# Performance work log

Hardware: AMD Instinct MI355X
Metric: run time of the kernel (lower is better)

Reference implementation:

```python
import jax, jax.numpy as jnp
import numpy as np

B, S, D, H, DH, F = 4, 2048, 1024, 16, 64, 4096
EPS = 1e-5


def setup_inputs() -> dict:
    key = jax.random.key(0)
    ks = jax.random.split(key, 8)
    std = 0.02
    return {
        "src": jax.random.normal(ks[0], (B, S, D), dtype=jnp.float32),
        # per-head Q/K/V projections, stacked: [H, D, DH]
        "Wq": jax.random.normal(ks[1], (H, D, DH), dtype=jnp.float32) * std,
        "bq": jnp.zeros((H, DH), dtype=jnp.float32),
        "Wk": jax.random.normal(ks[2], (H, D, DH), dtype=jnp.float32) * std,
        "bk": jnp.zeros((H, DH), dtype=jnp.float32),
        "Wv": jax.random.normal(ks[3], (H, D, DH), dtype=jnp.float32) * std,
        "bv": jnp.zeros((H, DH), dtype=jnp.float32),
        "Wo": jax.random.normal(ks[4], (H * DH, D), dtype=jnp.float32) * std,
        "bo": jnp.zeros((D,), dtype=jnp.float32),
        "ln1_w": jnp.ones((D,), dtype=jnp.float32),
        "ln1_b": jnp.zeros((D,), dtype=jnp.float32),
        "W1": jax.random.normal(ks[5], (D, F), dtype=jnp.float32) * std,
        "b1": jnp.zeros((F,), dtype=jnp.float32),
        "W2": jax.random.normal(ks[6], (F, D), dtype=jnp.float32) * std,
        "b2": jnp.zeros((D,), dtype=jnp.float32),
        "ln2_w": jnp.ones((D,), dtype=jnp.float32),
        "ln2_b": jnp.zeros((D,), dtype=jnp.float32),
    }


def _layernorm(x, w, b):
    m = jnp.mean(x, axis=-1, keepdims=True)
    v = jnp.mean(jnp.square(x - m), axis=-1, keepdims=True)
    return (x - m) * jax.lax.rsqrt(v + EPS) * w + b


def reference(src, Wq, bq, Wk, bk, Wv, bv, Wo, bo, ln1_w, ln1_b, W1, b1, W2, b2, ln2_w, ln2_b):
    # Per-head projections, batched over heads: [B,H,S,DH]
    q = jnp.einsum('bsd,hde->bhse', src, Wq) + bq[None, :, None, :]
    k = jnp.einsum('bsd,hde->bhse', src, Wk) + bk[None, :, None, :]
    v = jnp.einsum('bsd,hde->bhse', src, Wv) + bv[None, :, None, :]
    scale = jnp.asarray(DH, src.dtype) ** 0.5
    scores = jnp.einsum('bhqe,bhke->bhqk', q, k) / scale  # [B,H,S,S]
    attn = jax.nn.softmax(scores, axis=-1)
    ctx = jnp.einsum('bhqk,bhke->bhqe', attn, v)  # [B,H,S,DH]
    # concat heads along feature dim (matches torch.cat over head outputs)
    ctx = ctx.transpose(0, 2, 1, 3).reshape(src.shape[0], src.shape[1], H * DH)
    attn_out = ctx @ Wo + bo
    x = _layernorm(src + attn_out, ln1_w, ln1_b)
    ffn = jax.nn.relu(x @ W1 + b1) @ W2 + b2
    return _layernorm(x + ffn, ln2_w, ln2_b)
```

## Files before the change

kernel.cpp:

```cpp
#include <hip/hip_runtime.h>
#include <stdint.h>


typedef unsigned short u16;
typedef __attribute__((ext_vector_type(8))) short short8;
typedef __attribute__((ext_vector_type(4))) float f32x4;
typedef __attribute__((ext_vector_type(16))) float f32x16;

__device__ __forceinline__ u16 f2bf(float f) {
  union { float f; unsigned u; } v; v.f = f;
  unsigned r = (v.u + 0x7fffu + ((v.u >> 16) & 1u)) >> 16;
  return (u16)r;
}

__device__ __forceinline__ void gl_lds16(const u16* g, u16* l) {
  __builtin_amdgcn_global_load_lds(
      (const __attribute__((address_space(1))) unsigned int*)g,
      (__attribute__((address_space(3))) unsigned int*)l, 16, 0, 0);
}

__device__ __forceinline__ unsigned cvtpk(float lo, float hi) {
  unsigned r;
  asm("v_cvt_pk_bf16_f32 %0, %1, %2" : "=v"(r) : "v"(lo), "v"(hi));
  return r;
}
__device__ __forceinline__ void pl32_swap(unsigned& a, unsigned& b) {
  asm("v_permlane32_swap_b32 %0, %1" : "+v"(a), "+v"(b));
}


__global__ __launch_bounds__(256) void transpose_cast(const float* __restrict__ W,
                                                      u16* __restrict__ WT,
                                                      int K, int N) {
  __shared__ u16 T[64 * 72];
  const int tid = threadIdx.x;
  const long n0 = (long)blockIdx.x * 64, k0 = (long)blockIdx.y * 64;
#pragma unroll
  for (int i = 0; i < 4; i++) {
    int c = tid + i * 256;
    int kr = c >> 4, nc = (c & 15) * 4;
    float4 v = *(const float4*)(W + (k0 + kr) * N + n0 + nc);
    T[(nc + 0) * 72 + kr] = f2bf(v.x);
    T[(nc + 1) * 72 + kr] = f2bf(v.y);
    T[(nc + 2) * 72 + kr] = f2bf(v.z);
    T[(nc + 3) * 72 + kr] = f2bf(v.w);
  }
  __syncthreads();
#pragma unroll
  for (int i = 0; i < 2; i++) {
    int c = tid + i * 256;
    int nr = c >> 3, kc = (c & 7) * 8;
    *(uint4*)(WT + (n0 + nr) * K + k0 + kc) = *(const uint4*)(T + nr * 72 + kc);
  }
}

__global__ __launch_bounds__(256) void transpose_cast_qkv(const float* __restrict__ Wq,
                                                          const float* __restrict__ Wk,
                                                          const float* __restrict__ Wv,
                                                          u16* __restrict__ WT) {
  __shared__ u16 T[64 * 72];
  const int tid = threadIdx.x;
  const int n0 = blockIdx.x * 64, k0 = blockIdx.y * 64;
  const float* W = (n0 < 1024) ? Wq : (n0 < 2048 ? Wk : Wv);
  const int h = (n0 & 1023) >> 6;
#pragma unroll
  for (int i = 0; i < 4; i++) {
    int c = tid + i * 256;
    int kr = c >> 4, ec = (c & 15) * 4;
    float4 v = *(const float4*)(W + ((long)h * 1024 + k0 + kr) * 64 + ec);
    T[(ec + 0) * 72 + kr] = f2bf(v.x);
    T[(ec + 1) * 72 + kr] = f2bf(v.y);
    T[(ec + 2) * 72 + kr] = f2bf(v.z);
    T[(ec + 3) * 72 + kr] = f2bf(v.w);
  }
  __syncthreads();
#pragma unroll
  for (int i = 0; i < 2; i++) {
    int c = tid + i * 256;
    int nr = c >> 3, kc = (c & 7) * 8;
    *(uint4*)(WT + ((long)(n0 + nr)) * 1024 + k0 + kc) = *(const uint4*)(T + nr * 72 + kc);
  }
}

__global__ __launch_bounds__(256) void cast_bf16(const float* __restrict__ x, u16* __restrict__ y) {
  const long i = ((long)blockIdx.x * 256 + threadIdx.x) * 8;
  float4 a = *(const float4*)(x + i);
  float4 b = *(const float4*)(x + i + 4);
  uint4 o;
  o.x = (unsigned)f2bf(a.x) | ((unsigned)f2bf(a.y) << 16);
  o.y = (unsigned)f2bf(a.z) | ((unsigned)f2bf(a.w) << 16);
  o.z = (unsigned)f2bf(b.x) | ((unsigned)f2bf(b.y) << 16);
  o.w = (unsigned)f2bf(b.z) | ((unsigned)f2bf(b.w) << 16);
  *(uint4*)(y + i) = o;
}

__global__ __launch_bounds__(256) void build_bcat(const float* __restrict__ bq,
                                                  const float* __restrict__ bk,
                                                  const float* __restrict__ bv,
                                                  float* __restrict__ bcat) {
  int i = blockIdx.x * 256 + threadIdx.x;
  const float* s = (i < 1024) ? bq : (i < 2048 ? bk : bv);
  bcat[i] = s[i & 1023];
}

#define GEMM_SETUP                                                                 \
  __shared__ __align__(16) u16 Bs[2][4096];                                        \
  const int tid = threadIdx.x;                                                     \
  const int wave = tid >> 6, lane = tid & 63, quad = lane >> 4, l15 = lane & 15;   \
  const int wm = (wave >> 1) * 64, wn = (wave & 1) * 64;                           \
  const int id = blockIdx.x, xcd = id & 7, ii = id >> 3;                           \
  const long m0 = (long)(xcd * 8 + (ii & 7)) * 128, n0 = (long)(ii >> 3) * 128;    \
  const int srow = tid >> 2, sc = (tid & 3) ^ ((srow >> 1) & 3);                   \
  const u16* Bg = B + (n0 + srow) * K + sc * 8;                                    \
  const int cq = quad ^ ((l15 >> 1) & 3);                                          \
  const u16* Ap = A + (m0 + wm + l15) * K + quad * 8;                              \
  f32x4 acc[4][4] = {};

#define GEMM_KLOOP                                                                 \
  gl_lds16(Bg, &Bs[0][tid * 8]);                                                   \
  gl_lds16(Bg + (long)64 * K, &Bs[0][tid * 8 + 2048]);                             \
  short8 afc[4], afn[4];                                                           \
  _Pragma("unroll") for (int t = 0; t < 4; t++)                                    \
      afc[t] = *(const short8*)(Ap + (long)t * 16 * K);                            \
  for (int k0 = 0; k0 < K; k0 += 32) {                                             \
    __syncthreads();    \
    const int cur = (k0 >> 5) & 1;                                                 \
    if (k0 + 32 < K) {                                                             \
      gl_lds16(Bg + k0 + 32, &Bs[cur ^ 1][tid * 8]);                               \
      gl_lds16(Bg + (long)64 * K + k0 + 32, &Bs[cur ^ 1][tid * 8 + 2048]);         \
      _Pragma("unroll") for (int t = 0; t < 4; t++)                                \
          afn[t] = *(const short8*)(Ap + (long)t * 16 * K + k0 + 32);              \
    }                                                                              \
    short8 bfr[4];                                                                 \
    _Pragma("unroll") for (int t = 0; t < 4; t++)                                  \
        bfr[t] = *(const short8*)(&Bs[cur][(wn + t * 16 + l15) * 32 + cq * 8]);    \
    _Pragma("unroll") for (int i = 0; i < 4; i++)                                  \
        _Pragma("unroll") for (int j = 0; j < 4; j++)                              \
            acc[i][j] = __builtin_amdgcn_mfma_f32_16x16x32_bf16(afc[i], bfr[j],    \
                                                                acc[i][j], 0, 0, 0); \
    if (k0 + 32 < K) {                                                             \
      _Pragma("unroll") for (int t = 0; t < 4; t++) afc[t] = afn[t];               \
    }                                                                              \
  }

template <int MODE>
__global__ __launch_bounds__(256) void gemm_bt(const u16* __restrict__ A, const u16* __restrict__ B,
                                               const float* __restrict__ bias, void* __restrict__ Cout,
                                               int K, int N) {
  GEMM_SETUP
  float bb[4];
#pragma unroll
  for (int j = 0; j < 4; j++) bb[j] = bias[n0 + wn + j * 16 + l15];
  GEMM_KLOOP
#pragma unroll
  for (int i = 0; i < 4; i++) {
#pragma unroll
    for (int j = 0; j < 4; j++) {
      const long col = n0 + wn + j * 16 + l15;
      const long rowb = m0 + wm + i * 16 + quad * 4;
#pragma unroll
      for (int r = 0; r < 4; r++) {
        float v = acc[i][j][r] + bb[j];
        if (MODE == 2) v = fmaxf(v, 0.f);
        if (MODE == 0)
          ((float*)Cout)[(rowb + r) * N + col] = v;
        else
          ((u16*)Cout)[(rowb + r) * N + col] = f2bf(v);
      }
    }
  }
}

template <int MODE>
__global__ __launch_bounds__(512) void gemm_bt_sk(const u16* __restrict__ A, const u16* __restrict__ B,
                                                  const float* __restrict__ bias, void* __restrict__ Cout,
                                                  int K, int N) {
  __shared__ __align__(16) u16 As[2][2][4096];
  __shared__ __align__(16) u16 Bs[2][2][4096];
  const int tid = threadIdx.x;
  const int wave = tid >> 6, lane = tid & 63, quad = lane >> 4, l15 = lane & 15;
  const int kh = wave >> 2, w4 = wave & 3;
  const int wm = (w4 >> 1) * 64, wn = (w4 & 1) * 64;
  const int id = blockIdx.x, xcd = id & 7, ii = id >> 3;
  const long m0 = (long)(xcd * 8 + (ii & 7)) * 128, n0 = (long)(ii >> 3) * 128;
  const int t = tid & 255;
  const int srow = t >> 2, sc = (t & 3) ^ ((srow >> 1) & 3);
  const int Kh = K >> 1;
  const u16* Ag = A + (m0 + srow) * K + kh * Kh + sc * 8;
  const u16* Bg = B + (n0 + srow) * K + kh * Kh + sc * 8;
  const int cx = (l15 >> 1) & 3;
  f32x4 acc[4][4] = {};
  gl_lds16(Ag, &As[kh][0][t * 8]);
  gl_lds16(Ag + (long)64 * K, &As[kh][0][t * 8 + 2048]);
  gl_lds16(Bg, &Bs[kh][0][t * 8]);
  gl_lds16(Bg + (long)64 * K, &Bs[kh][0][t * 8 + 2048]);
  for (int k0 = 0; k0 < Kh; k0 += 32) {
    __syncthreads();
    const int cur = (k0 >> 5) & 1;
    if (k0 + 32 < Kh) {
      gl_lds16(Ag + k0 + 32, &As[kh][cur ^ 1][t * 8]);
      gl_lds16(Ag + (long)64 * K + k0 + 32, &As[kh][cur ^ 1][t * 8 + 2048]);
      gl_lds16(Bg + k0 + 32, &Bs[kh][cur ^ 1][t * 8]);
      gl_lds16(Bg + (long)64 * K + k0 + 32, &Bs[kh][cur ^ 1][t * 8 + 2048]);
    }
    short8 af[4], bfr[4];
#pragma unroll
    for (int tt = 0; tt < 4; tt++)
      af[tt] = *(const short8*)(&As[kh][cur][(wm + tt * 16 + l15) * 32 + (quad ^ cx) * 8]);
#pragma unroll
    for (int tt = 0; tt < 4; tt++)
      bfr[tt] = *(const short8*)(&Bs[kh][cur][(wn + tt * 16 + l15) * 32 + (quad ^ cx) * 8]);
#pragma unroll
    for (int i = 0; i < 4; i++)
#pragma unroll
      for (int j = 0; j < 4; j++)
        acc[i][j] = __builtin_amdgcn_mfma_f32_16x16x32_bf16(af[i], bfr[j], acc[i][j], 0, 0, 0);
  }
  __syncthreads();
  float* red = (w4 & 2) ? (float*)Bs : (float*)As;
  float* myred = red + (w4 & 1) * 4096 + lane * 4;
  if (kh == 1) {
#pragma unroll
    for (int i = 0; i < 4; i++)
#pragma unroll
      for (int j = 0; j < 4; j++)
        *(f32x4*)(myred + (i * 4 + j) * 256) = acc[i][j];
  }
  __syncthreads();
  if (kh == 0) {
#pragma unroll
    for (int i = 0; i < 4; i++) {
#pragma unroll
      for (int j = 0; j < 4; j++) {
        const f32x4 o = *(const f32x4*)(myred + (i * 4 + j) * 256);
        const long col = n0 + wn + j * 16 + l15;
        const float bb = bias[col];
        const long rowb = m0 + wm + i * 16 + quad * 4;
#pragma unroll
        for (int r = 0; r < 4; r++) {
          float v = acc[i][j][r] + o[r] + bb;
          if (MODE == 2) v = fmaxf(v, 0.f);
          if (MODE == 0)
            ((float*)Cout)[(rowb + r) * N + col] = v;
          else
            ((u16*)Cout)[(rowb + r) * N + col] = f2bf(v);
        }
      }
    }
  }
}

__global__ __launch_bounds__(256) void gemm_qkv(const u16* __restrict__ A, const u16* __restrict__ B,
                                                const float* __restrict__ bias,
                                                u16* __restrict__ QKb, u16* __restrict__ Vt, int K) {
  GEMM_SETUP
  float bb[4];
#pragma unroll
  for (int j = 0; j < 4; j++) bb[j] = bias[n0 + wn + j * 16 + l15];
  GEMM_KLOOP
#pragma unroll
  for (int i = 0; i < 4; i++) {
#pragma unroll
    for (int j = 0; j < 4; j++) {
      const int col0 = (int)n0 + wn + j * 16;
      const int col = col0 + l15;
      const long rowb = m0 + wm + i * 16 + quad * 4;
      if (col0 < 1024) {
#pragma unroll
        for (int r = 0; r < 4; r++)
          QKb[(rowb + r) * 2048 + col] = f2bf((acc[i][j][r] + bb[j]) * 0.1803368801f);
      } else if (col0 < 2048) {
#pragma unroll
        for (int r = 0; r < 4; r++)
          QKb[(rowb + r) * 2048 + col] = f2bf(acc[i][j][r] + bb[j]);
      } else {
        const int ec = col - 2048;
        const int bq = (int)(rowb >> 11), s = (int)(rowb & 2047);
        uint2 p;
        p.x = (unsigned)f2bf(acc[i][j][0] + bb[j]) | ((unsigned)f2bf(acc[i][j][1] + bb[j]) << 16);
        p.y = (unsigned)f2bf(acc[i][j][2] + bb[j]) | ((unsigned)f2bf(acc[i][j][3] + bb[j]) << 16);
        *(uint2*)(Vt + ((long)(bq * 16 + (ec >> 6)) * 64 + (ec & 63)) * 2048 + s) = p;
      }
    }
  }
}


__device__ __forceinline__ void stage_tile(const u16* __restrict__ g, u16* __restrict__ lds, int tid) {
#pragma unroll
  for (int i = 0; i < 2; i++) {
    const int s = i * 256 + tid;
    const int r = s >> 3, cs = s & 7;
    const int c = cs ^ (r & 7);
    gl_lds16(g + (long)r * 2048 + c * 8, lds + s * 8);
  }
}
__device__ __forceinline__ short8 frag(const u16* __restrict__ buf, int row, int chunk) {
  const int slot = row * 8 + (chunk ^ (row & 7));
  return *(const short8*)(buf + slot * 8);
}

__global__ __launch_bounds__(256, 2) void flash_attn(const u16* __restrict__ QKb,
                                                     const u16* __restrict__ Vt,
                                                     u16* __restrict__ ctx) {
  __shared__ __align__(16) u16 Kbuf[2][4096];
  __shared__ __align__(16) u16 Vbuf[2][4096];
  const int tid = threadIdx.x, wave = tid >> 6, lane = tid & 63;
  const int l31 = lane & 31, hi = lane >> 5;
  const int bh = blockIdx.x, b = bh >> 4, h = bh & 15;
  const int qt = blockIdx.y;
  const long qbase = (long)b * 2048 + qt * 256 + wave * 64;
  const u16* Qg = QKb + qbase * 2048 + h * 64;
  const u16* Kg = QKb + ((long)b * 2048) * 2048 + 1024 + h * 64;
  const u16* Vg = Vt + (long)bh * 64 * 2048;

  short8 qf[2][4];
#pragma unroll
  for (int j = 0; j < 2; j++)
#pragma unroll
    for (int ks = 0; ks < 4; ks++)
      qf[j][ks] = *(const short8*)(Qg + (long)(j * 32 + l31) * 2048 + ks * 16 + hi * 8);

  f32x16 O[2][2] = {};
  float rs[2] = {0.f, 0.f};

  stage_tile(Kg, Kbuf[0], tid);
  stage_tile(Vg, Vbuf[0], tid);

  for (int kt = 0; kt < 32; kt++) {
    __syncthreads();
    if (kt < 31) {
      stage_tile(Kg + (long)(kt + 1) * 64 * 2048, Kbuf[(kt + 1) & 1], tid);
      stage_tile(Vg + (kt + 1) * 64, Vbuf[(kt + 1) & 1], tid);
    }
    const u16* Kb = Kbuf[kt & 1];
    const u16* Vb = Vbuf[kt & 1];

#pragma unroll
    for (int m = 0; m < 2; m++) {
      short8 ak[4];
#pragma unroll
      for (int ks = 0; ks < 4; ks++) ak[ks] = frag(Kb, m * 32 + l31, ks * 2 + hi);
      f32x16 S[2] = {};
#pragma unroll
      for (int ks = 0; ks < 4; ks++)
#pragma unroll
        for (int j = 0; j < 2; j++)
          S[j] = __builtin_amdgcn_mfma_f32_32x32x16_bf16(ak[ks], qf[j][ks], S[j], 0, 0, 0);

      short8 pf[2][2];
#pragma unroll
      for (int j = 0; j < 2; j++) {
#pragma unroll
        for (int r = 0; r < 16; r++) S[j][r] = __builtin_amdgcn_exp2f(S[j][r]);
        rs[j] += ((S[j][0] + S[j][1]) + (S[j][2] + S[j][3])) +
                 ((S[j][4] + S[j][5]) + (S[j][6] + S[j][7])) +
                 ((S[j][8] + S[j][9]) + (S[j][10] + S[j][11])) +
                 ((S[j][12] + S[j][13]) + (S[j][14] + S[j][15]));
        unsigned w0 = cvtpk(S[j][0], S[j][1]), w1 = cvtpk(S[j][2], S[j][3]);
        unsigned w2 = cvtpk(S[j][4], S[j][5]), w3 = cvtpk(S[j][6], S[j][7]);
        unsigned w4 = cvtpk(S[j][8], S[j][9]), w5 = cvtpk(S[j][10], S[j][11]);
        unsigned w6 = cvtpk(S[j][12], S[j][13]), w7 = cvtpk(S[j][14], S[j][15]);
        pl32_swap(w2, w0); pl32_swap(w3, w1);
        pl32_swap(w6, w4); pl32_swap(w7, w5);
        union { unsigned u[4]; short8 s8; } f0, f1;
        f0.u[0] = w0; f0.u[1] = w1; f0.u[2] = w2; f0.u[3] = w3;
        f1.u[0] = w4; f1.u[1] = w5; f1.u[2] = w6; f1.u[3] = w7;
        pf[j][0] = f0.s8; pf[j][1] = f1.s8;
      }

#pragma unroll
      for (int et = 0; et < 2; et++) {
        short8 av[2];
#pragma unroll
        for (int ks2 = 0; ks2 < 2; ks2++)
          av[ks2] = frag(Vb, et * 32 + l31, m * 4 + ks2 * 2 + hi);
#pragma unroll
        for (int j = 0; j < 2; j++)
#pragma unroll
          for (int ks2 = 0; ks2 < 2; ks2++)
            O[et][j] = __builtin_amdgcn_mfma_f32_32x32x16_bf16(av[ks2], pf[j][ks2],
                                                               O[et][j], 0, 0, 0);
      }
    }
  }

#pragma unroll
  for (int j = 0; j < 2; j++) rs[j] += __shfl_xor(rs[j], 32);
#pragma unroll
  for (int j = 0; j < 2; j++) {
    const float inv = 1.f / rs[j];
    const long row = qbase + j * 32 + l31;
#pragma unroll
    for (int et = 0; et < 2; et++)
#pragma unroll
      for (int g = 0; g < 4; g++) {
        const int e0 = et * 32 + g * 8 + hi * 4;
        uint2 p;
        p.x = (unsigned)f2bf(O[et][j][g * 4 + 0] * inv) |
              ((unsigned)f2bf(O[et][j][g * 4 + 1] * inv) << 16);
        p.y = (unsigned)f2bf(O[et][j][g * 4 + 2] * inv) |
              ((unsigned)f2bf(O[et][j][g * 4 + 3] * inv) << 16);
        *(uint2*)(ctx + row * 1024 + h * 64 + e0) = p;
      }
  }
}

template <bool WB>
__global__ __launch_bounds__(256) void add_ln(const float* __restrict__ a, const float* __restrict__ c,
                                              const float* __restrict__ w, const float* __restrict__ bias,
                                              float* __restrict__ xout, u16* __restrict__ xbf) {
  const int row = blockIdx.x, tid = threadIdx.x;
  const long off = (long)row * 1024 + tid * 4;
  float4 va = *(const float4*)(a + off);
  float4 vc = *(const float4*)(c + off);
  float4 s = {va.x + vc.x, va.y + vc.y, va.z + vc.z, va.w + vc.w};
  float sum = s.x + s.y + s.z + s.w;
  float sq = s.x * s.x + s.y * s.y + s.z * s.z + s.w * s.w;
#pragma unroll
  for (int o = 32; o > 0; o >>= 1) {
    sum += __shfl_xor(sum, o);
    sq += __shfl_xor(sq, o);
  }
  __shared__ float red[8];
  const int wave = tid >> 6;
  if ((tid & 63) == 0) { red[wave] = sum; red[wave + 4] = sq; }
  __syncthreads();
  sum = red[0] + red[1] + red[2] + red[3];
  sq = red[4] + red[5] + red[6] + red[7];
  const float mean = sum * (1.f / 1024.f);
  const float var = sq * (1.f / 1024.f) - mean * mean;
  const float rstd = rsqrtf(var + 1e-5f);
  float4 vw = *(const float4*)(w + tid * 4);
  float4 vb = *(const float4*)(bias + tid * 4);
  float4 y;
  y.x = (s.x - mean) * rstd * vw.x + vb.x;
  y.y = (s.y - mean) * rstd * vw.y + vb.y;
  y.z = (s.z - mean) * rstd * vw.z + vb.z;
  y.w = (s.w - mean) * rstd * vw.w + vb.w;
  *(float4*)(xout + off) = y;
  if (WB) {
    uint2 o2;
    o2.x = (unsigned)f2bf(y.x) | ((unsigned)f2bf(y.y) << 16);
    o2.y = (unsigned)f2bf(y.z) | ((unsigned)f2bf(y.w) << 16);
    *(uint2*)(xbf + off) = o2;
  }
}

extern "C" void kernel_launch(void* const* d_in, const int* in_sizes, int n_in,
                              void* d_out, int out_size, void* d_ws, size_t ws_size,
                              hipStream_t stream) {
  (void)in_sizes; (void)n_in; (void)out_size; (void)ws_size;
  const float* src = (const float*)d_in[0];
  const float* Wq = (const float*)d_in[1];
  const float* bq = (const float*)d_in[2];
  const float* Wk = (const float*)d_in[3];
  const float* bk = (const float*)d_in[4];
  const float* Wv = (const float*)d_in[5];
  const float* bv = (const float*)d_in[6];
  const float* Wo = (const float*)d_in[7];
  const float* bo = (const float*)d_in[8];
  const float* ln1w = (const float*)d_in[9];
  const float* ln1b = (const float*)d_in[10];
  const float* W1 = (const float*)d_in[11];
  const float* b1 = (const float*)d_in[12];
  const float* W2 = (const float*)d_in[13];
  const float* b2 = (const float*)d_in[14];
  const float* ln2w = (const float*)d_in[15];
  const float* ln2b = (const float*)d_in[16];

  char* ws = (char*)d_ws;
  u16* WqkvT = (u16*)(ws + 0);
  u16* WoT = (u16*)(ws + (6ul << 20));
  u16* W1T = (u16*)(ws + (8ul << 20));
  u16* W2T = (u16*)(ws + (16ul << 20));
  float* bcat = (float*)(ws + (24ul << 20));
  u16* srcb = (u16*)(ws + (25ul << 20));
  u16* QKb = (u16*)(ws + (41ul << 20));
  u16* Vt = (u16*)(ws + (73ul << 20));
  u16* ctxb = (u16*)(ws + (89ul << 20));
  float* x = (float*)(ws + (105ul << 20));
  u16* xb = (u16*)(ws + (137ul << 20));
  u16* hb = (u16*)(ws + (41ul << 20));
  float* out = (float*)d_out;

  transpose_cast_qkv<<<dim3(48, 16), 256, 0, stream>>>(Wq, Wk, Wv, WqkvT);
  transpose_cast<<<dim3(16, 16), 256, 0, stream>>>(Wo, WoT, 1024, 1024);
  transpose_cast<<<dim3(64, 16), 256, 0, stream>>>(W1, W1T, 1024, 4096);
  transpose_cast<<<dim3(16, 64), 256, 0, stream>>>(W2, W2T, 4096, 1024);
  cast_bf16<<<4096, 256, 0, stream>>>(src, srcb);
  build_bcat<<<12, 256, 0, stream>>>(bq, bk, bv, bcat);

  gemm_qkv<<<24 * 64, 256, 0, stream>>>(srcb, WqkvT, bcat, QKb, Vt, 1024);
  flash_attn<<<dim3(64, 8), 256, 0, stream>>>(QKb, Vt, ctxb);
  gemm_bt_sk<0><<<8 * 64, 512, 0, stream>>>(ctxb, WoT, bo, out, 1024, 1024);
  add_ln<true><<<8192, 256, 0, stream>>>(src, out, ln1w, ln1b, x, xb);
  gemm_bt<2><<<32 * 64, 256, 0, stream>>>(xb, W1T, b1, hb, 1024, 4096);
  gemm_bt_sk<0><<<8 * 64, 512, 0, stream>>>(hb, W2T, b2, out, 4096, 1024);
  add_ln<false><<<8192, 256, 0, stream>>>(x, out, ln2w, ln2b, out, nullptr);
}
```

Before: 600.8 us.

## Stage A tiles in LDS and enlarge QKV/FFN1 GEMM tiles to 256x128

The QKV projection and FFN1 GEMMs now stage both A and B tiles into LDS through async global-to-LDS loads, instead of each wave reading its A fragments directly from global memory. Each block computes a 256x128 output tile with every wave owning 64 rows by 128 columns (4x8 MFMA accumulators), which halves the grid size. The goal is more data reuse per load and fewer uncoalesced global reads of A. In exchange it uses more LDS and accumulator registers, which may lower occupancy, and the smaller grid gives fewer blocks per CU.

Result: no change. 607.1 us (+1.0%).

```diff
diff --git a/kernel.cpp b/kernel.cpp
--- a/kernel.cpp
+++ b/kernel.cpp
@@ -103,61 +103,59 @@
   bcat[i] = s[i & 1023];
 }
 
-#define GEMM_SETUP                                                                 \
-  __shared__ __align__(16) u16 Bs[2][4096];                                        \
+#define GEMM2_SETUP                                                                \
+  __shared__ __align__(16) u16 As[2][8192];                    \
+  __shared__ __align__(16) u16 Bs[2][4096];                    \
   const int tid = threadIdx.x;                                                     \
   const int wave = tid >> 6, lane = tid & 63, quad = lane >> 4, l15 = lane & 15;   \
-  const int wm = (wave >> 1) * 64, wn = (wave & 1) * 64;                           \
   const int id = blockIdx.x, xcd = id & 7, ii = id >> 3;                           \
-  const long m0 = (long)(xcd * 8 + (ii & 7)) * 128, n0 = (long)(ii >> 3) * 128;    \
-  const int srow = tid >> 2, sc = (tid & 3) ^ ((srow >> 1) & 3);                   \
-  const u16* Bg = B + (n0 + srow) * K + sc * 8;                                    \
+  const long m0 = (long)(xcd * 4 + (ii & 3)) * 256, n0 = (long)(ii >> 2) * 128;    \
+  const int tr = tid >> 2, sc = (tid & 3) ^ ((tr >> 1) & 3);                       \
+  const u16* Ag = A + (m0 + tr) * K + sc * 8;                                      \
+  const u16* Bg = B + (n0 + tr) * K + sc * 8;                                      \
   const int cq = quad ^ ((l15 >> 1) & 3);                                          \
-  const u16* Ap = A + (m0 + wm + l15) * K + quad * 8;                              \
-  f32x4 acc[4][4] = {};
-
-#define GEMM_KLOOP                                                                 \
-  gl_lds16(Bg, &Bs[0][tid * 8]);                                                   \
-  gl_lds16(Bg + (long)64 * K, &Bs[0][tid * 8 + 2048]);                             \
-  short8 afc[4], afn[4];                                                           \
-  _Pragma("unroll") for (int t = 0; t < 4; t++)                                    \
-      afc[t] = *(const short8*)(Ap + (long)t * 16 * K);                            \
+  f32x4 acc[4][8] = {};
+
+#define G2_STAGE(buf, kof)                                                         \
+  {                                                                                \
+    _Pragma("unroll") for (int p = 0; p < 4; p++)                                  \
+        gl_lds16(Ag + (long)(p * 64) * K + (kof), &As[buf][(p * 256 + tid) * 8]);  \
+    _Pragma("unroll") for (int p = 0; p < 2; p++)                                  \
+        gl_lds16(Bg + (long)(p * 64) * K + (kof), &Bs[buf][(p * 256 + tid) * 8]);  \
+  }
+
+#define GEMM2_KLOOP                                                                \
+  G2_STAGE(0, 0)                                                                   \
   for (int k0 = 0; k0 < K; k0 += 32) {                                             \
-    __syncthreads();    \
+    __syncthreads();         \
     const int cur = (k0 >> 5) & 1;                                                 \
-    if (k0 + 32 < K) {                                                             \
-      gl_lds16(Bg + k0 + 32, &Bs[cur ^ 1][tid * 8]);                               \
-      gl_lds16(Bg + (long)64 * K + k0 + 32, &Bs[cur ^ 1][tid * 8 + 2048]);         \
-      _Pragma("unroll") for (int t = 0; t < 4; t++)                                \
-          afn[t] = *(const short8*)(Ap + (long)t * 16 * K + k0 + 32);              \
-    }                                                                              \
-    short8 bfr[4];                                                                 \
+    if (k0 + 32 < K) G2_STAGE(cur ^ 1, k0 + 32)                                    \
+    short8 af[4], bfr[8];                                                          \
     _Pragma("unroll") for (int t = 0; t < 4; t++)                                  \
-        bfr[t] = *(const short8*)(&Bs[cur][(wn + t * 16 + l15) * 32 + cq * 8]);    \
+        af[t] = *(const short8*)(&As[cur][(wave * 64 + t * 16 + l15) * 32 + cq * 8]); \
+    _Pragma("unroll") for (int j = 0; j < 8; j++)                                  \
+        bfr[j] = *(const short8*)(&Bs[cur][(j * 16 + l15) * 32 + cq * 8]);         \
     _Pragma("unroll") for (int i = 0; i < 4; i++)                                  \
-        _Pragma("unroll") for (int j = 0; j < 4; j++)                              \
-            acc[i][j] = __builtin_amdgcn_mfma_f32_16x16x32_bf16(afc[i], bfr[j],    \
+        _Pragma("unroll") for (int j = 0; j < 8; j++)                              \
+            acc[i][j] = __builtin_amdgcn_mfma_f32_16x16x32_bf16(af[i], bfr[j],     \
                                                                 acc[i][j], 0, 0, 0); \
-    if (k0 + 32 < K) {                                                             \
-      _Pragma("unroll") for (int t = 0; t < 4; t++) afc[t] = afn[t];               \
-    }                                                                              \
   }
 
 template <int MODE>
-__global__ __launch_bounds__(256) void gemm_bt(const u16* __restrict__ A, const u16* __restrict__ B,
-                                               const float* __restrict__ bias, void* __restrict__ Cout,
-                                               int K, int N) {
-  GEMM_SETUP
-  float bb[4];
-#pragma unroll
-  for (int j = 0; j < 4; j++) bb[j] = bias[n0 + wn + j * 16 + l15];
-  GEMM_KLOOP
+__global__ __launch_bounds__(256) void gemm_bt2(const u16* __restrict__ A, const u16* __restrict__ B,
+                                                const float* __restrict__ bias, void* __restrict__ Cout,
+                                                int K, int N) {
+  GEMM2_SETUP
+  float bb[8];
+#pragma unroll
+  for (int j = 0; j < 8; j++) bb[j] = bias[n0 + j * 16 + l15];
+  GEMM2_KLOOP
 #pragma unroll
   for (int i = 0; i < 4; i++) {
 #pragma unroll
-    for (int j = 0; j < 4; j++) {
-      const long col = n0 + wn + j * 16 + l15;
-      const long rowb = m0 + wm + i * 16 + quad * 4;
+    for (int j = 0; j < 8; j++) {
+      const long col = n0 + j * 16 + l15;
+      const long rowb = m0 + wave * 64 + i * 16 + quad * 4;
 #pragma unroll
       for (int r = 0; r < 4; r++) {
         float v = acc[i][j][r] + bb[j];
@@ -166,6 +164,41 @@
           ((float*)Cout)[(rowb + r) * N + col] = v;
         else
           ((u16*)Cout)[(rowb + r) * N + col] = f2bf(v);
+      }
+    }
+  }
+}
+
+__global__ __launch_bounds__(256) void gemm_qkv2(const u16* __restrict__ A, const u16* __restrict__ B,
+                                                 const float* __restrict__ bias,
+                                                 u16* __restrict__ QKb, u16* __restrict__ Vt, int K) {
+  GEMM2_SETUP
+  float bb[8];
+#pragma unroll
+  for (int j = 0; j < 8; j++) bb[j] = bias[n0 + j * 16 + l15];
+  GEMM2_KLOOP
+#pragma unroll
+  for (int i = 0; i < 4; i++) {
+#pragma unroll
+    for (int j = 0; j < 8; j++) {
+      const int col0 = (int)n0 + j * 16;
+      const int col = col0 + l15;
+      const long rowb = m0 + wave * 64 + i * 16 + quad * 4;
+      if (col0 < 1024) {
+#pragma unroll
+        for (int r = 0; r < 4; r++)
+          QKb[(rowb + r) * 2048 + col] = f2bf((acc[i][j][r] + bb[j]) * 0.1803368801f);
+      } else if (col0 < 2048) {
+#pragma unroll
+        for (int r = 0; r < 4; r++)
+          QKb[(rowb + r) * 2048 + col] = f2bf(acc[i][j][r] + bb[j]);
+      } else {
+        const int ec = col - 2048;
+        const int bq = (int)(rowb >> 11), s = (int)(rowb & 2047);
+        uint2 p;
+        p.x = (unsigned)f2bf(acc[i][j][0] + bb[j]) | ((unsigned)f2bf(acc[i][j][1] + bb[j]) << 16);
+        p.y = (unsigned)f2bf(acc[i][j][2] + bb[j]) | ((unsigned)f2bf(acc[i][j][3] + bb[j]) << 16);
+        *(uint2*)(Vt + ((long)(bq * 16 + (ec >> 6)) * 64 + (ec & 63)) * 2048 + s) = p;
       }
     }
   }
@@ -250,41 +283,6 @@
   }
 }
 
-__global__ __launch_bounds__(256) void gemm_qkv(const u16* __restrict__ A, const u16* __restrict__ B,
-                                                const float* __restrict__ bias,
-                                                u16* __restrict__ QKb, u16* __restrict__ Vt, int K) {
-  GEMM_SETUP
-  float bb[4];
-#pragma unroll
-  for (int j = 0; j < 4; j++) bb[j] = bias[n0 + wn + j * 16 + l15];
-  GEMM_KLOOP
-#pragma unroll
-  for (int i = 0; i < 4; i++) {
-#pragma unroll
-    for (int j = 0; j < 4; j++) {
-      const int col0 = (int)n0 + wn + j * 16;
-      const int col = col0 + l15;
-      const long rowb = m0 + wm + i * 16 + quad * 4;
-      if (col0 < 1024) {
-#pragma unroll
-        for (int r = 0; r < 4; r++)
-          QKb[(rowb + r) * 2048 + col] = f2bf((acc[i][j][r] + bb[j]) * 0.1803368801f);
-      } else if (col0 < 2048) {
-#pragma unroll
-        for (int r = 0; r < 4; r++)
-          QKb[(rowb + r) * 2048 + col] = f2bf(acc[i][j][r] + bb[j]);
-      } else {
-        const int ec = col - 2048;
-        const int bq = (int)(rowb >> 11), s = (int)(rowb & 2047);
-        uint2 p;
-        p.x = (unsigned)f2bf(acc[i][j][0] + bb[j]) | ((unsigned)f2bf(acc[i][j][1] + bb[j]) << 16);
-        p.y = (unsigned)f2bf(acc[i][j][2] + bb[j]) | ((unsigned)f2bf(acc[i][j][3] + bb[j]) << 16);
-        *(uint2*)(Vt + ((long)(bq * 16 + (ec >> 6)) * 64 + (ec & 63)) * 2048 + s) = p;
-      }
-    }
-  }
-}
-
 
 __device__ __forceinline__ void stage_tile(const u16* __restrict__ g, u16* __restrict__ lds, int tid) {
 #pragma unroll
@@ -491,11 +489,11 @@
   cast_bf16<<<4096, 256, 0, stream>>>(src, srcb);
   build_bcat<<<12, 256, 0, stream>>>(bq, bk, bv, bcat);
 
-  gemm_qkv<<<24 * 64, 256, 0, stream>>>(srcb, WqkvT, bcat, QKb, Vt, 1024);
+  gemm_qkv2<<<24 * 32, 256, 0, stream>>>(srcb, WqkvT, bcat, QKb, Vt, 1024);
   flash_attn<<<dim3(64, 8), 256, 0, stream>>>(QKb, Vt, ctxb);
   gemm_bt_sk<0><<<8 * 64, 512, 0, stream>>>(ctxb, WoT, bo, out, 1024, 1024);
   add_ln<true><<<8192, 256, 0, stream>>>(src, out, ln1w, ln1b, x, xb);
-  gemm_bt<2><<<32 * 64, 256, 0, stream>>>(xb, W1T, b1, hb, 1024, 4096);
+  gemm_bt2<2><<<32 * 32, 256, 0, stream>>>(xb, W1T, b1, hb, 1024, 4096);
   gemm_bt_sk<0><<<8 * 64, 512, 0, stream>>>(hb, W2T, b2, out, 4096, 1024);
   add_ln<false><<<8192, 256, 0, stream>>>(x, out, ln2w, ln2b, out, nullptr);
 }
```
